# Performance work log

Measured on AMD Instinct MI355X. Metric: run time of the kernel, lower is better.

## Reference

```python
import jax, jax.numpy as jnp
import numpy as np

EMBED_DIM = 1024
N_HEADS = 16
HEAD_DIM = EMBED_DIM // N_HEADS

def setup_inputs() -> dict:
    key = jax.random.key(0)
    kx, kq, kk, kv, ko = jax.random.split(key, 5)
    s = 1.0 / np.sqrt(EMBED_DIM)
    return {
        "x": jax.random.normal(kx, (4, 2048, EMBED_DIM), dtype=jnp.float32),
        "Wq": jax.random.normal(kq, (EMBED_DIM, EMBED_DIM), dtype=jnp.float32) * s,
        "Wk": jax.random.normal(kk, (EMBED_DIM, EMBED_DIM), dtype=jnp.float32) * s,
        "Wv": jax.random.normal(kv, (EMBED_DIM, EMBED_DIM), dtype=jnp.float32) * s,
        "Wo": jax.random.normal(ko, (EMBED_DIM, EMBED_DIM), dtype=jnp.float32) * s,
    }

def reference(x, Wq, Wk, Wv, Wo):
    B, T, D = x.shape
    H, Dh = N_HEADS, HEAD_DIM
    # projections (nn.Linear: y = x @ W.T); split heads -> [B, H, T, Dh]
    Q = (x @ Wq.T).reshape(B, T, H, Dh).transpose(0, 2, 1, 3)
    K = (x @ Wk.T).reshape(B, T, H, Dh).transpose(0, 2, 1, 3)
    V = (x @ Wv.T).reshape(B, T, H, Dh).transpose(0, 2, 1, 3)
    scores = jnp.einsum("bhqd,bhkd->bhqk", Q, K) / jnp.sqrt(jnp.float32(Dh))
    attn = jax.nn.softmax(scores, axis=-1)
    out = jnp.einsum("bhqk,bhkd->bhqd", attn, V)  # [B,H,T,Dh]
    out = out.transpose(0, 2, 1, 3).reshape(B, T, D)
    return out @ Wo.T
```

## Files before the change

### kernel.cpp

```cpp
#include <hip/hip_runtime.h>

typedef _Float16 f16;
typedef _Float16 f16x8 __attribute__((ext_vector_type(8)));
typedef _Float16 f16x4 __attribute__((ext_vector_type(4)));
typedef float f32x4 __attribute__((ext_vector_type(4)));

#define MFMA16(a, b, c) __builtin_amdgcn_mfma_f32_16x16x32_f16((a), (b), (c), 0, 0, 0)
#define MEMBAR() __asm__ __volatile__("" ::: "memory")

__device__ __forceinline__ void cp16(const f16* g, f16* l) {
  __builtin_amdgcn_global_load_lds(
      (const __attribute__((address_space(1))) void*)g,
      (__attribute__((address_space(3))) void*)l, 16, 0, 0);
}

__global__ __launch_bounds__(256) void cvt_all(
    const float* __restrict__ x,  const float* __restrict__ Wq,
    const float* __restrict__ Wk, const float* __restrict__ Wv,
    const float* __restrict__ Wo,
    f16* __restrict__ X16, f16* __restrict__ Wq16, f16* __restrict__ Wk16,
    f16* __restrict__ Wv16, f16* __restrict__ Wo16) {
  int blk = blockIdx.x;
  const float* src; f16* dst; size_t off;
  if (blk < 4096) { src = x; dst = X16; off = (size_t)blk * 2048; }
  else {
    int t = blk - 4096, widx = t >> 9, loc = t & 511;
    src = (widx == 0) ? Wq : (widx == 1) ? Wk : (widx == 2) ? Wv : Wo;
    dst = (widx == 0) ? Wq16 : (widx == 1) ? Wk16 : (widx == 2) ? Wv16 : Wo16;
    off = (size_t)loc * 2048;
  }
  size_t e = off + (size_t)threadIdx.x * 8;
  const float4* s = (const float4*)(src + e);
  float4 a = s[0], b = s[1];
  f16x8 o;
  o[0] = (f16)a.x; o[1] = (f16)a.y; o[2] = (f16)a.z; o[3] = (f16)a.w;
  o[4] = (f16)b.x; o[5] = (f16)b.y; o[6] = (f16)b.z; o[7] = (f16)b.w;
  *(f16x8*)(dst + e) = o;
}

__device__ __forceinline__ void gemm_core(
    const f16* __restrict__ A, const f16* __restrict__ B, void* __restrict__ Cv,
    bool outF16, int N, int K, int bm, int bn, float scale, f16* As, f16* Bs) {
  const int tid = threadIdx.x;
  const int lane = tid & 63, w = tid >> 6;
  const int wm = w >> 1, wn = w & 1;
  const int c = lane & 15, q = lane >> 4;
  const int key = (c >> 1) & 3;
  f32x4 acc[4][4] = {};

  const int Lrow = lane >> 2, Lp = (lane & 3) ^ ((lane >> 3) & 3);
  auto stage = [&](int k0, int bufi) {
#pragma unroll
    for (int j = 0; j < 2; ++j) {
      int r0 = (w * 2 + j) * 16;
      cp16(A + (size_t)(bm + r0 + Lrow) * K + k0 + Lp * 8,
           As + bufi * 4096 + r0 * 32 + lane * 8);
    }
#pragma unroll
    for (int j = 0; j < 2; ++j) {
      int r0 = (w * 2 + j) * 16;
      cp16(B + (size_t)(bn + r0 + Lrow) * K + k0 + Lp * 8,
           Bs + bufi * 4096 + r0 * 32 + lane * 8);
    }
  };

  stage(0, 0);
  const int NIT = K >> 5;
  for (int i = 0; i < NIT; ++i) {
    if (i + 1 < NIT) {
      stage((i + 1) << 5, (i + 1) & 1);
      __builtin_amdgcn_s_waitcnt(0x0F74);
    } else {
      __builtin_amdgcn_s_waitcnt(0x0F70);
    }
    __builtin_amdgcn_s_barrier();
    MEMBAR();
    const f16* Ab = As + (i & 1) * 4096;
    const f16* Bb = Bs + (i & 1) * 4096;
    f16x8 af[4], bf[4];
#pragma unroll
    for (int mt = 0; mt < 4; ++mt)
      af[mt] = *(const f16x8*)(Ab + (wm * 64 + mt * 16 + c) * 32 + (q ^ key) * 8);
#pragma unroll
    for (int nt = 0; nt < 4; ++nt)
      bf[nt] = *(const f16x8*)(Bb + (wn * 64 + nt * 16 + c) * 32 + (q ^ key) * 8);
#pragma unroll
    for (int mt = 0; mt < 4; ++mt)
#pragma unroll
      for (int nt = 0; nt < 4; ++nt)
        acc[mt][nt] = MFMA16(af[mt], bf[nt], acc[mt][nt]);
    MEMBAR();
    __builtin_amdgcn_s_barrier();
  }

#pragma unroll
  for (int mt = 0; mt < 4; ++mt)
#pragma unroll
    for (int nt = 0; nt < 4; ++nt)
#pragma unroll
      for (int r = 0; r < 4; ++r) {
        size_t row = bm + wm * 64 + mt * 16 + q * 4 + r;
        size_t col = bn + wn * 64 + nt * 16 + c;
        float v = acc[mt][nt][r] * scale;
        if (outF16) ((f16*)Cv)[row * N + col] = (f16)v;
        else ((float*)Cv)[row * N + col] = v;
      }
}

__global__ __launch_bounds__(256, 4) void gemm_qkvt(
    const f16* __restrict__ X, const f16* __restrict__ Wq,
    const f16* __restrict__ Wk, const f16* __restrict__ Wv,
    f16* __restrict__ Q, f16* __restrict__ Ko, f16* __restrict__ VT, float cs) {
  __shared__ __align__(16) f16 As[8192], Bs[8192];
  const int z = blockIdx.z, x = blockIdx.x;
  if (z < 2) {
    gemm_core(X, z ? Wk : Wq, z ? (void*)Ko : (void*)Q, true, 1024, 1024,
              (x >> 3) * 128, (x & 7) * 128, z ? 1.0f : cs, As, Bs);
  } else {
    gemm_core(Wv, X, (void*)VT, true, 8192, 1024,
              (x >> 6) * 128, (x & 63) * 128, 1.0f, As, Bs);
  }
}

__global__ __launch_bounds__(256, 4) void gemm_o(
    const f16* __restrict__ A, const f16* __restrict__ Wo, float* __restrict__ out) {
  __shared__ __align__(16) f16 As[8192], Bs[8192];
  const int x = blockIdx.x;
  gemm_core(A, Wo, (void*)out, false, 1024, 1024,
            (x >> 3) * 128, (x & 7) * 128, 1.0f, As, Bs);
}

__global__ __launch_bounds__(512, 4) void attn_kernel(
    const f16* __restrict__ Qg, const f16* __restrict__ Kg,
    const f16* __restrict__ VTg, f16* __restrict__ Og) {
  const int T = 2048, D = 1024;
  const int x = blockIdx.x;
  const int xcd = x & 7, rem = x >> 3;
  const int qt = rem & 7, grp = rem >> 3;
  const int bh = (grp << 3) | xcd;
  const int b = bh >> 4, h = bh & 15;
  const size_t base = ((size_t)b * T) * D + h * 64;
  const size_t baseV = (size_t)h * 64 * 8192 + (size_t)b * T;
  __shared__ __align__(16) f16 smem[32768];
  const int tid = threadIdx.x;
  const int lane = tid & 63, w = tid >> 6;
  const int c = lane & 15, q = lane >> 4;
  const int cx = c & 7;
  f16* Kb = smem;
  f16* Vb = smem + 8192;
  f16* Ps = smem + 16384 + w * 2048;

#pragma unroll
  for (int j = 0; j < 4; ++j) {
    int cb = (w * 4 + j) * 64;
    int ch = cb + lane;
    int row = ch >> 3, p = (ch & 7) ^ (row & 7);
    cp16(Qg + base + (size_t)(qt * 256 + row) * D + p * 8, smem + cb * 8);
  }
  __syncthreads();
  f16x8 qf[2][2];
#pragma unroll
  for (int nt = 0; nt < 2; ++nt)
#pragma unroll
    for (int kh = 0; kh < 2; ++kh)
      qf[nt][kh] = *(const f16x8*)(smem + (w * 32 + nt * 16 + c) * 64 + ((kh * 4 + q) ^ cx) * 8);
  __syncthreads();

  float l_[2] = {0.f, 0.f};
  f32x4 o_[2][4] = {};

  auto stageKV = [&](int kv, int bufi) {
    f16* Ks = Kb + bufi * 4096;
    f16* Vt = Vb + bufi * 4096;
    int cb = w * 64;
    int ch = cb + lane;
    int row = ch >> 3, p = (ch & 7) ^ (row & 7);
    cp16(Kg + base + (size_t)(kv + row) * D + p * 8, Ks + cb * 8);
    cp16(VTg + baseV + (size_t)row * 8192 + kv + p * 8, Vt + cb * 8);
  };

  stageKV(0, 0);
  for (int i = 0; i < 32; ++i) {
    if (i < 31) {
      stageKV((i + 1) * 64, (i + 1) & 1);
      __builtin_amdgcn_s_waitcnt(0x0F72);
    } else {
      __builtin_amdgcn_s_waitcnt(0x0F70);
    }
    __builtin_amdgcn_s_barrier();
    f16* Ks = Kb + (i & 1) * 4096;
    f16* Vt = Vb + (i & 1) * 4096;

    f32x4 st[4][2] = {};
#pragma unroll
    for (int kh = 0; kh < 2; ++kh) {
      f16x8 kf[4];
#pragma unroll
      for (int mt = 0; mt < 4; ++mt)
        kf[mt] = *(const f16x8*)(Ks + (mt * 16 + c) * 64 + ((kh * 4 + q) ^ cx) * 8);
      __builtin_amdgcn_s_setprio(1);
#pragma unroll
      for (int mt = 0; mt < 4; ++mt)
#pragma unroll
        for (int g = 0; g < 2; ++g)
          st[mt][g] = MFMA16(kf[mt], qf[g][kh], st[mt][g]);
      __builtin_amdgcn_s_setprio(0);
    }

#pragma unroll
    for (int g = 0; g < 2; ++g) {
      float s = 0.f;
#pragma unroll
      for (int mt = 0; mt < 4; ++mt) {
        float p0 = __builtin_amdgcn_exp2f(st[mt][g][0]);
        float p1 = __builtin_amdgcn_exp2f(st[mt][g][1]);
        float p2 = __builtin_amdgcn_exp2f(st[mt][g][2]);
        float p3 = __builtin_amdgcn_exp2f(st[mt][g][3]);
        s += (p0 + p1) + (p2 + p3);
        f16x4 pv;
        pv[0] = (f16)p0; pv[1] = (f16)p1; pv[2] = (f16)p2; pv[3] = (f16)p3;
        *(f16x4*)(Ps + g * 1024 + c * 64 + ((mt * 2 + (q >> 1)) ^ cx) * 8 + (q & 1) * 4) = pv;
      }
      s += __shfl_xor(s, 16);
      s += __shfl_xor(s, 32);
      l_[g] += s;
    }

    MEMBAR();
    __builtin_amdgcn_s_setprio(1);
#pragma unroll
    for (int kc = 0; kc < 2; ++kc) {
      f16x8 pf0 = *(const f16x8*)(Ps + c * 64 + ((kc * 4 + q) ^ cx) * 8);
      f16x8 pf1 = *(const f16x8*)(Ps + 1024 + c * 64 + ((kc * 4 + q) ^ cx) * 8);
#pragma unroll
      for (int d = 0; d < 4; ++d) {
        f16x8 vf = *(const f16x8*)(Vt + (d * 16 + c) * 64 + ((kc * 4 + q) ^ cx) * 8);
        o_[0][d] = MFMA16(pf0, vf, o_[0][d]);
        o_[1][d] = MFMA16(pf1, vf, o_[1][d]);
      }
    }
    __builtin_amdgcn_s_setprio(0);
    MEMBAR();
    __builtin_amdgcn_s_barrier();
  }

#pragma unroll
  for (int g = 0; g < 2; ++g)
#pragma unroll
    for (int r = 0; r < 4; ++r) {
      float linv = 1.0f / __shfl(l_[g], q * 4 + r);
      size_t row = (size_t)qt * 256 + w * 32 + g * 16 + q * 4 + r;
#pragma unroll
      for (int d = 0; d < 4; ++d)
        Og[base + row * D + d * 16 + c] = (f16)(o_[g][d][r] * linv);
    }
}

extern "C" void kernel_launch(void* const* d_in, const int* in_sizes, int n_in,
                              void* d_out, int out_size, void* d_ws, size_t ws_size,
                              hipStream_t stream) {
  const float* x  = (const float*)d_in[0];
  const float* Wq = (const float*)d_in[1];
  const float* Wk = (const float*)d_in[2];
  const float* Wv = (const float*)d_in[3];
  const float* Wo = (const float*)d_in[4];
  char* ws = (char*)d_ws;
  const size_t MB = 1ull << 20;
  f16* X16  = (f16*)(ws + 0 * MB);
  f16* Wq16 = (f16*)(ws + 16 * MB);
  f16* Wk16 = (f16*)(ws + 18 * MB);
  f16* Wv16 = (f16*)(ws + 20 * MB);
  f16* Wo16 = (f16*)(ws + 22 * MB);
  f16* Q16  = (f16*)(ws + 24 * MB);
  f16* K16  = (f16*)(ws + 40 * MB);
  f16* VT16 = (f16*)(ws + 56 * MB);
  f16* A16  = (f16*)(ws + 72 * MB);

  const float cs = 0.18033688011112042f;

  cvt_all<<<6144, 256, 0, stream>>>(x, Wq, Wk, Wv, Wo,
                                    X16, Wq16, Wk16, Wv16, Wo16);

  gemm_qkvt<<<dim3(512, 1, 3), 256, 0, stream>>>(
      X16, Wq16, Wk16, Wv16, Q16, K16, VT16, cs);

  attn_kernel<<<dim3(512, 1, 1), 512, 0, stream>>>(Q16, K16, VT16, A16);

  gemm_o<<<512, 256, 0, stream>>>(A16, Wo16, (float*)d_out);
}
```

Before: 267.9 us.

## Keep softmax probabilities in registers by permuting V^T columns in projection epilogue

```diff
diff --git a/kernel.cpp b/kernel.cpp
--- a/kernel.cpp
+++ b/kernel.cpp
@@ -40,7 +40,8 @@
 
 __device__ __forceinline__ void gemm_core(
     const f16* __restrict__ A, const f16* __restrict__ B, void* __restrict__ Cv,
-    bool outF16, int N, int K, int bm, int bn, float scale, f16* As, f16* Bs) {
+    bool outF16, bool permT, int N, int K, int bm, int bn, float scale,
+    f16* As, f16* Bs) {
   const int tid = threadIdx.x;
   const int lane = tid & 63, w = tid >> 6;
   const int wm = w >> 1, wn = w & 1;
@@ -101,6 +102,11 @@
       for (int r = 0; r < 4; ++r) {
         size_t row = bm + wm * 64 + mt * 16 + q * 4 + r;
         size_t col = bn + wn * 64 + nt * 16 + c;
+        if (permT) {
+          int t = (int)col & 63;
+          col = (col & ~(size_t)63) |
+                (size_t)((t & 0x23) | ((t & 0x0C) << 1) | ((t & 0x10) >> 2));
+        }
         float v = acc[mt][nt][r] * scale;
         if (outF16) ((f16*)Cv)[row * N + col] = (f16)v;
         else ((float*)Cv)[row * N + col] = v;
@@ -114,10 +120,10 @@
   __shared__ __align__(16) f16 As[8192], Bs[8192];
   const int z = blockIdx.z, x = blockIdx.x;
   if (z < 2) {
-    gemm_core(X, z ? Wk : Wq, z ? (void*)Ko : (void*)Q, true, 1024, 1024,
+    gemm_core(X, z ? Wk : Wq, z ? (void*)Ko : (void*)Q, true, false, 1024, 1024,
               (x >> 3) * 128, (x & 7) * 128, z ? 1.0f : cs, As, Bs);
   } else {
-    gemm_core(Wv, X, (void*)VT, true, 8192, 1024,
+    gemm_core(Wv, X, (void*)VT, true, true, 8192, 1024,
               (x >> 6) * 128, (x & 63) * 128, 1.0f, As, Bs);
   }
 }
@@ -126,11 +132,11 @@
     const f16* __restrict__ A, const f16* __restrict__ Wo, float* __restrict__ out) {
   __shared__ __align__(16) f16 As[8192], Bs[8192];
   const int x = blockIdx.x;
-  gemm_core(A, Wo, (void*)out, false, 1024, 1024,
+  gemm_core(A, Wo, (void*)out, false, false, 1024, 1024,
             (x >> 3) * 128, (x & 7) * 128, 1.0f, As, Bs);
 }
 
-__global__ __launch_bounds__(512, 4) void attn_kernel(
+__global__ __launch_bounds__(512, 6) void attn_kernel(
     const f16* __restrict__ Qg, const f16* __restrict__ Kg,
     const f16* __restrict__ VTg, f16* __restrict__ Og) {
   const int T = 2048, D = 1024;
@@ -141,14 +147,13 @@
   const int b = bh >> 4, h = bh & 15;
   const size_t base = ((size_t)b * T) * D + h * 64;
   const size_t baseV = (size_t)h * 64 * 8192 + (size_t)b * T;
-  __shared__ __align__(16) f16 smem[32768];
+  __shared__ __align__(16) f16 smem[16384];
   const int tid = threadIdx.x;
   const int lane = tid & 63, w = tid >> 6;
   const int c = lane & 15, q = lane >> 4;
   const int cx = c & 7;
   f16* Kb = smem;
   f16* Vb = smem + 8192;
-  f16* Ps = smem + 16384 + w * 2048;
 
 #pragma unroll
   for (int j = 0; j < 4; ++j) {
@@ -188,6 +193,7 @@
       __builtin_amdgcn_s_waitcnt(0x0F70);
     }
     __builtin_amdgcn_s_barrier();
+
     f16* Ks = Kb + (i & 1) * 4096;
     f16* Vt = Vb + (i & 1) * 4096;
 
@@ -207,6 +213,7 @@
       __builtin_amdgcn_s_setprio(0);
     }
 
+    f16x8 pf[2][2];
 #pragma unroll
     for (int g = 0; g < 2; ++g) {
       float s = 0.f;
@@ -217,31 +224,31 @@
         float p2 = __builtin_amdgcn_exp2f(st[mt][g][2]);
         float p3 = __builtin_amdgcn_exp2f(st[mt][g][3]);
         s += (p0 + p1) + (p2 + p3);
-        f16x4 pv;
-        pv[0] = (f16)p0; pv[1] = (f16)p1; pv[2] = (f16)p2; pv[3] = (f16)p3;
-        *(f16x4*)(Ps + g * 1024 + c * 64 + ((mt * 2 + (q >> 1)) ^ cx) * 8 + (q & 1) * 4) = pv;
+        int kc = mt >> 1, hh = (mt & 1) * 4;
+        pf[g][kc][hh + 0] = (f16)p0; pf[g][kc][hh + 1] = (f16)p1;
+        pf[g][kc][hh + 2] = (f16)p2; pf[g][kc][hh + 3] = (f16)p3;
       }
-      s += __shfl_xor(s, 16);
-      s += __shfl_xor(s, 32);
       l_[g] += s;
     }
 
-    MEMBAR();
     __builtin_amdgcn_s_setprio(1);
 #pragma unroll
-    for (int kc = 0; kc < 2; ++kc) {
-      f16x8 pf0 = *(const f16x8*)(Ps + c * 64 + ((kc * 4 + q) ^ cx) * 8);
-      f16x8 pf1 = *(const f16x8*)(Ps + 1024 + c * 64 + ((kc * 4 + q) ^ cx) * 8);
+    for (int kc = 0; kc < 2; ++kc)
 #pragma unroll
       for (int d = 0; d < 4; ++d) {
         f16x8 vf = *(const f16x8*)(Vt + (d * 16 + c) * 64 + ((kc * 4 + q) ^ cx) * 8);
-        o_[0][d] = MFMA16(pf0, vf, o_[0][d]);
-        o_[1][d] = MFMA16(pf1, vf, o_[1][d]);
+        o_[0][d] = MFMA16(pf[0][kc], vf, o_[0][d]);
+        o_[1][d] = MFMA16(pf[1][kc], vf, o_[1][d]);
       }
-    }
     __builtin_amdgcn_s_setprio(0);
     MEMBAR();
     __builtin_amdgcn_s_barrier();
+  }
+
+#pragma unroll
+  for (int g = 0; g < 2; ++g) {
+    l_[g] += __shfl_xor(l_[g], 16);
+    l_[g] += __shfl_xor(l_[g], 32);
   }
 
 #pragma unroll
```

Result: slower. 555.2 us (+107.3%).
